# Optimization experiments

Measured on AMD Instinct MI355X. Metric: run time of the kernel, lower is better.

## Reference

```python
import jax, jax.numpy as jnp
import numpy as np

BS, QLEN, DIM, NH = 2, 2048, 1024, 16
HD = DIM // NH


def setup_inputs() -> dict:
    key = jax.random.key(0)
    ks = jax.random.split(key, 6)
    std = 0.02
    return {
        "x": jax.random.normal(ks[0], (BS, QLEN, DIM), dtype=jnp.float32),
        "mask": jnp.ones((BS, QLEN), dtype=jnp.float32),
        "Wq": jax.random.normal(ks[1], (DIM, DIM), dtype=jnp.float32) * std,
        "bq": jnp.zeros((DIM,), dtype=jnp.float32),
        "Wk": jax.random.normal(ks[2], (DIM, DIM), dtype=jnp.float32) * std,
        "bk": jnp.zeros((DIM,), dtype=jnp.float32),
        "Wv": jax.random.normal(ks[3], (DIM, DIM), dtype=jnp.float32) * std,
        "bv": jnp.zeros((DIM,), dtype=jnp.float32),
        "Wo": jax.random.normal(ks[4], (DIM, DIM), dtype=jnp.float32) * std,
        "bo": jnp.zeros((DIM,), dtype=jnp.float32),
    }


def reference(x, mask, Wq, bq, Wk, bk, Wv, bv, Wo, bo):
    bs, qlen, dim = x.shape
    # project and split heads: [bs, nh, len, hd]
    def split_heads(t):
        return t.reshape(bs, -1, NH, HD).transpose(0, 2, 1, 3)

    q = split_heads(x @ Wq + bq) / jnp.sqrt(jnp.float32(HD))
    k = split_heads(x @ Wk + bk)
    v = split_heads(x @ Wv + bv)

    scores = jnp.einsum("bhqd,bhkd->bhqk", q, k)  # [bs, nh, qlen, klen]
    m = mask.reshape(bs, 1, 1, -1)  # 2D mask -> broadcast over heads and q
    scores = scores - 1e30 * (1.0 - m)
    weights = jax.nn.softmax(scores, axis=-1)
    # dropout p=0.0 at inference -> no-op; head_mask is None
    context = jnp.einsum("bhqk,bhkd->bhqd", weights, v)
    context = context.transpose(0, 2, 1, 3).reshape(bs, qlen, NH * HD)
    return context @ Wo + bo
```

## Files before the change

kernel.cpp:

```cpp
#include <hip/hip_runtime.h>
#include <stdint.h>

#define BSZ  2
#define SEQ  2048
#define DIM  1024
#define NHD  16
#define HD   64
#define MTOT (BSZ*SEQ)

using short8  = __attribute__((ext_vector_type(8))) short;
using floatx4 = __attribute__((ext_vector_type(4))) float;

#define QSCALE 0.18033688011112042f
#define BIGM   1.44e30f

__device__ __forceinline__ unsigned short f2bf(float f) {
    unsigned int u = __float_as_uint(f);
    u += 0x7fffu + ((u >> 16) & 1u);
    return (unsigned short)(u >> 16);
}
__device__ __forceinline__ unsigned int pk2r(float a, float b) {
    unsigned int ua = __float_as_uint(a) + 0x8000u;
    unsigned int ub = __float_as_uint(b) + 0x8000u;
    return __builtin_amdgcn_perm(ub, ua, 0x07060302);
}

__device__ __forceinline__ void gll16(const void* g, const void* lds) {
    unsigned int loff = (unsigned int)(unsigned long long)lds;
    __builtin_amdgcn_global_load_lds(
        (const __attribute__((address_space(1))) unsigned int*)g,
        (__attribute__((address_space(3))) unsigned int*)loff, 16, 0, 0);
}

__global__ __launch_bounds__(256)
void conv_x(const float* __restrict__ X, unsigned short* __restrict__ Xbf) {
    size_t i = ((size_t)blockIdx.x * 256 + threadIdx.x) * 8;
    float4 a = *(const float4*)(X + i);
    float4 b = *(const float4*)(X + i + 4);
    uint4 u = {pk2r(a.x, a.y), pk2r(a.z, a.w), pk2r(b.x, b.y), pk2r(b.z, b.w)};
    *(uint4*)(Xbf + i) = u;
}

__global__ __launch_bounds__(256)
void conv_wt(const float* __restrict__ Wq, const float* __restrict__ Wk,
             const float* __restrict__ Wv, const float* __restrict__ Wo,
             unsigned short* __restrict__ Wt3, unsigned short* __restrict__ Wto)
{
    __shared__ float tile[64 * 65];
    const int z = blockIdx.z;
    const float* W = (z == 0) ? Wq : (z == 1) ? Wk : (z == 2) ? Wv : Wo;
    unsigned short* out = (z < 3) ? (Wt3 + (size_t)z * DIM * DIM) : Wto;
    const int k0 = blockIdx.x * 64, n0 = blockIdx.y * 64;
    const int t = threadIdx.x;
    const int r = t >> 2, c0 = (t & 3) * 16;
#pragma unroll
    for (int j = 0; j < 4; ++j) {
        float4 v = *(const float4*)&W[(size_t)(k0 + r) * DIM + n0 + c0 + j * 4];
        tile[r * 65 + c0 + j * 4 + 0] = v.x;
        tile[r * 65 + c0 + j * 4 + 1] = v.y;
        tile[r * 65 + c0 + j * 4 + 2] = v.z;
        tile[r * 65 + c0 + j * 4 + 3] = v.w;
    }
    __syncthreads();
    unsigned int p[8];
#pragma unroll
    for (int j = 0; j < 8; ++j)
        p[j] = pk2r(tile[(c0 + 2 * j) * 65 + r], tile[(c0 + 2 * j + 1) * 65 + r]);
    uint4 u0 = {p[0], p[1], p[2], p[3]}, u1 = {p[4], p[5], p[6], p[7]};
    unsigned short* dst = out + (size_t)(n0 + r) * DIM + k0 + c0;
    *(uint4*)dst = u0;
    *(uint4*)(dst + 8) = u1;
}

__global__ __launch_bounds__(256)
void qkv_gemm(const unsigned short* __restrict__ Xbf,
              const unsigned short* __restrict__ Wt3,
              const float* __restrict__ bq, const float* __restrict__ bk,
              const float* __restrict__ bv,
              unsigned short* __restrict__ Qb,
              unsigned short* __restrict__ Kb,
              unsigned short* __restrict__ VbT)
{
    __shared__ unsigned short As[128 * 32];
    __shared__ unsigned short Bs[128 * 32];

    const int t = threadIdx.x, w = t >> 6, lane = t & 63;
    const int lm = lane & 15, grp = lane >> 4;
    const int wm = w >> 1, wn = w & 1;
    const int m0 = blockIdx.x * 128;
    const int mat = blockIdx.y >> 3;
    const int n0 = (blockIdx.y & 7) * 128;
    const unsigned short* Bg = Wt3 + (size_t)mat * DIM * DIM;

    const int lr = lane >> 2, lc = (lane & 3) * 8;

    floatx4 acc[4][4];
#pragma unroll
    for (int i = 0; i < 4; ++i)
#pragma unroll
        for (int j = 0; j < 4; ++j) acc[i][j] = (floatx4){0.f, 0.f, 0.f, 0.f};

    for (int kt = 0; kt < DIM / 32; ++kt) {
        const int k0 = kt * 32;
        const int r0 = w * 16;
        gll16(Xbf + (size_t)(m0 + r0 + lr) * DIM + k0 + lc,      &As[r0 * 32]);
        gll16(Xbf + (size_t)(m0 + 64 + r0 + lr) * DIM + k0 + lc, &As[(64 + r0) * 32]);
        gll16(Bg  + (size_t)(n0 + r0 + lr) * DIM + k0 + lc,      &Bs[r0 * 32]);
        gll16(Bg  + (size_t)(n0 + 64 + r0 + lr) * DIM + k0 + lc, &Bs[(64 + r0) * 32]);
        __syncthreads();
        short8 af[4], bf[4];
#pragma unroll
        for (int mt = 0; mt < 4; ++mt)
            af[mt] = *(const short8*)&As[(wm * 64 + mt * 16 + lm) * 32 + grp * 8];
#pragma unroll
        for (int nt = 0; nt < 4; ++nt)
            bf[nt] = *(const short8*)&Bs[(wn * 64 + nt * 16 + lm) * 32 + grp * 8];
#pragma unroll
        for (int mt = 0; mt < 4; ++mt)
#pragma unroll
            for (int nt = 0; nt < 4; ++nt)
                acc[mt][nt] = __builtin_amdgcn_mfma_f32_16x16x32_bf16(af[mt], bf[nt], acc[mt][nt], 0, 0, 0);
        __syncthreads();
    }

    if (mat == 2) {
#pragma unroll
        for (int nt = 0; nt < 4; ++nt) {
            const int c = n0 + wn * 64 + nt * 16 + lm;
            const float bb = bv[c];
            const int h = c >> 6, d = c & 63;
#pragma unroll
            for (int mt = 0; mt < 4; ++mt) {
                const int r = m0 + wm * 64 + mt * 16 + grp * 4;
                const int b = r >> 11, s = r & 2047;
                const int si = s & 63, sb = s & ~63;
                const int sphys = sb + ((((si >> 3) ^ (d & 7)) << 3) | (si & 7));
                uint2 pv;
                pv.x = pk2r(acc[mt][nt][0] + bb, acc[mt][nt][1] + bb);
                pv.y = pk2r(acc[mt][nt][2] + bb, acc[mt][nt][3] + bb);
                *(uint2*)&VbT[(((size_t)(b * NHD + h)) * HD + d) * SEQ + sphys] = pv;
            }
        }
    } else if (mat == 1) {
#pragma unroll
        for (int nt = 0; nt < 4; ++nt) {
            const int c = n0 + wn * 64 + nt * 16 + lm;
            const float bb = bk[c];
            const int h = c >> 6, d = c & 63;
#pragma unroll
            for (int mt = 0; mt < 4; ++mt)
#pragma unroll
                for (int reg = 0; reg < 4; ++reg) {
                    const int r = m0 + wm * 64 + mt * 16 + grp * 4 + reg;
                    const int b = r >> 11, s = r & 2047;
                    const int dphys = (((d >> 3) ^ (s & 7)) << 3) | (d & 7);
                    Kb[(((size_t)(b * NHD + h)) * SEQ + s) * HD + dphys] =
                        f2bf(acc[mt][nt][reg] + bb);
                }
        }
    } else {
#pragma unroll
        for (int nt = 0; nt < 4; ++nt) {
            const int c = n0 + wn * 64 + nt * 16 + lm;
            const float bb = bq[c];
            const int h = c >> 6, d = c & 63;
#pragma unroll
            for (int mt = 0; mt < 4; ++mt)
#pragma unroll
                for (int reg = 0; reg < 4; ++reg) {
                    const int r = m0 + wm * 64 + mt * 16 + grp * 4 + reg;
                    const int b = r >> 11, s = r & 2047;
                    Qb[(((size_t)(b * NHD + h)) * SEQ + s) * HD + d] =
                        f2bf((acc[mt][nt][reg] + bb) * QSCALE);
                }
        }
    }
}

__global__ __launch_bounds__(256)
void attn(const unsigned short* __restrict__ Qb,
          const unsigned short* __restrict__ Kb,
          const unsigned short* __restrict__ VbT,
          const float* __restrict__ mask,
          unsigned short* __restrict__ Cb)
{
    __shared__ unsigned short Kt[2][64 * 64];
    __shared__ unsigned short Vt[2][64 * 64];
    __shared__ unsigned short Ps[4][16 * 72];

    const int t = threadIdx.x, w = t >> 6, lane = t & 63;
    const int lm = lane & 15, grp = lane >> 4;
    const int x7 = lm & 7;
    const int bh = blockIdx.y, b = bh >> 4, h = bh & 15;
    const int q0 = blockIdx.x * 64;

    short8 qf[2];
    {
        const unsigned short* qrow = Qb + ((size_t)bh * SEQ + q0 + w * 16 + lm) * HD;
        qf[0] = *(const short8*)(qrow + grp * 8);
        qf[1] = *(const short8*)(qrow + 32 + grp * 8);
    }

    floatx4 oacc[4];
#pragma unroll
    for (int i = 0; i < 4; ++i) oacc[i] = (floatx4){0.f, 0.f, 0.f, 0.f};
    float lpart = 0.f;

    const unsigned short* Kg = Kb + (size_t)bh * SEQ * HD;
    const unsigned short* Vg = VbT + (size_t)bh * HD * SEQ;
    const int srow = lane >> 3, scol = (lane & 7) * 8;
    const float* maskb = mask + b * SEQ;
    unsigned short* Pw = &Ps[w][0];

    {
        gll16(Kg + (size_t)(0 * 64 + w * 16 + srow) * HD + scol,     &Kt[0][(w * 16) * 64]);
        gll16(Kg + (size_t)(0 * 64 + w * 16 + 8 + srow) * HD + scol, &Kt[0][(w * 16 + 8) * 64]);
        gll16(Vg + (size_t)(w * 16 + srow) * SEQ + 0 * 64 + scol,     &Vt[0][(w * 16) * 64]);
        gll16(Vg + (size_t)(w * 16 + 8 + srow) * SEQ + 0 * 64 + scol, &Vt[0][(w * 16 + 8) * 64]);
    }

    for (int kt = 0; kt < SEQ / 64; ++kt) {
        const int cur = kt & 1;
        __syncthreads();
        if (kt + 1 < SEQ / 64) {
            const int nxt = cur ^ 1, kn = kt + 1;
            gll16(Kg + (size_t)(kn * 64 + w * 16 + srow) * HD + scol,     &Kt[nxt][(w * 16) * 64]);
            gll16(Kg + (size_t)(kn * 64 + w * 16 + 8 + srow) * HD + scol, &Kt[nxt][(w * 16 + 8) * 64]);
            gll16(Vg + (size_t)(w * 16 + srow) * SEQ + kn * 64 + scol,     &Vt[nxt][(w * 16) * 64]);
            gll16(Vg + (size_t)(w * 16 + 8 + srow) * SEQ + kn * 64 + scol, &Vt[nxt][(w * 16 + 8) * 64]);
        }

        floatx4 sv[4];
#pragma unroll
        for (int cg = 0; cg < 4; ++cg) {
            short8 a0 = *(const short8*)&Kt[cur][(cg * 16 + lm) * 64 + ((grp    ) ^ x7) * 8];
            short8 a1 = *(const short8*)&Kt[cur][(cg * 16 + lm) * 64 + ((4 + grp) ^ x7) * 8];
            floatx4 s = (floatx4){0.f, 0.f, 0.f, 0.f};
            s = __builtin_amdgcn_mfma_f32_16x16x32_bf16(a0, qf[0], s, 0, 0, 0);
            s = __builtin_amdgcn_mfma_f32_16x16x32_bf16(a1, qf[1], s, 0, 0, 0);
            sv[cg] = s;
        }

#pragma unroll
        for (int cg = 0; cg < 4; ++cg) {
            float4 mv = *(const float4*)&maskb[kt * 64 + cg * 16 + grp * 4];
            float p0 = __builtin_exp2f(sv[cg][0] + __builtin_fmaf(mv.x, BIGM, -BIGM));
            float p1 = __builtin_exp2f(sv[cg][1] + __builtin_fmaf(mv.y, BIGM, -BIGM));
            float p2 = __builtin_exp2f(sv[cg][2] + __builtin_fmaf(mv.z, BIGM, -BIGM));
            float p3 = __builtin_exp2f(sv[cg][3] + __builtin_fmaf(mv.w, BIGM, -BIGM));
            lpart += (p0 + p1) + (p2 + p3);
            uint2 pk;
            pk.x = pk2r(p0, p1);
            pk.y = pk2r(p2, p3);
            *(uint2*)&Pw[lm * 72 + cg * 16 + grp * 4] = pk;
        }

#pragma unroll
        for (int s2 = 0; s2 < 2; ++s2) {
            short8 ap = *(const short8*)&Pw[lm * 72 + s2 * 32 + grp * 8];
#pragma unroll
            for (int dg = 0; dg < 4; ++dg) {
                short8 bv2 = *(const short8*)&Vt[cur][(dg * 16 + lm) * 64 + ((s2 * 4 + grp) ^ x7) * 8];
                oacc[dg] = __builtin_amdgcn_mfma_f32_16x16x32_bf16(ap, bv2, oacc[dg], 0, 0, 0);
            }
        }
    }

    lpart += __shfl_xor(lpart, 16);
    lpart += __shfl_xor(lpart, 32);
    const float linv = (lpart > 0.f) ? 1.0f / lpart : 0.f;
    float inv[4];
#pragma unroll
    for (int r = 0; r < 4; ++r) inv[r] = __shfl(linv, grp * 4 + r);
#pragma unroll
    for (int dg = 0; dg < 4; ++dg)
#pragma unroll
        for (int r = 0; r < 4; ++r) {
            const int s = q0 + w * 16 + grp * 4 + r;
            Cb[((size_t)(b * SEQ + s)) * DIM + h * HD + dg * 16 + lm] =
                f2bf(oacc[dg][r] * inv[r]);
        }
}

__global__ __launch_bounds__(256)
void out_gemm(const unsigned short* __restrict__ Cb,
              const unsigned short* __restrict__ Wto,
              const float* __restrict__ bo,
              float* __restrict__ out)
{
    __shared__ unsigned short As[128 * 32];
    __shared__ unsigned short Bs[64 * 32];

    const int t = threadIdx.x, w = t >> 6, lane = t & 63;
    const int lm = lane & 15, grp = lane >> 4;
    const int m0 = blockIdx.x * 128;
    const int n0 = blockIdx.y * 64;

    const int lr = lane >> 2, lc = (lane & 3) * 8;

    floatx4 acc[2][4];
#pragma unroll
    for (int i = 0; i < 2; ++i)
#pragma unroll
        for (int j = 0; j < 4; ++j) acc[i][j] = (floatx4){0.f, 0.f, 0.f, 0.f};

    for (int kt = 0; kt < DIM / 32; ++kt) {
        const int k0 = kt * 32;
        const int r0 = w * 16;
        gll16(Cb  + (size_t)(m0 + r0 + lr) * DIM + k0 + lc,      &As[r0 * 32]);
        gll16(Cb  + (size_t)(m0 + 64 + r0 + lr) * DIM + k0 + lc, &As[(64 + r0) * 32]);
        gll16(Wto + (size_t)(n0 + r0 + lr) * DIM + k0 + lc,      &Bs[r0 * 32]);
        __syncthreads();
        short8 af[2], bf[4];
#pragma unroll
        for (int mt = 0; mt < 2; ++mt)
            af[mt] = *(const short8*)&As[(w * 32 + mt * 16 + lm) * 32 + grp * 8];
#pragma unroll
        for (int nt = 0; nt < 4; ++nt)
            bf[nt] = *(const short8*)&Bs[(nt * 16 + lm) * 32 + grp * 8];
#pragma unroll
        for (int mt = 0; mt < 2; ++mt)
#pragma unroll
            for (int nt = 0; nt < 4; ++nt)
                acc[mt][nt] = __builtin_amdgcn_mfma_f32_16x16x32_bf16(af[mt], bf[nt], acc[mt][nt], 0, 0, 0);
        __syncthreads();
    }

#pragma unroll
    for (int nt = 0; nt < 4; ++nt) {
        const int c = n0 + nt * 16 + lm;
        const float bb = bo[c];
#pragma unroll
        for (int mt = 0; mt < 2; ++mt)
#pragma unroll
            for (int reg = 0; reg < 4; ++reg) {
                const int r = m0 + w * 32 + mt * 16 + grp * 4 + reg;
                out[(size_t)r * DIM + c] = acc[mt][nt][reg] + bb;
            }
    }
}

extern "C" void kernel_launch(void* const* d_in, const int* in_sizes, int n_in,
                              void* d_out, int out_size, void* d_ws, size_t ws_size,
                              hipStream_t stream)
{
    const float* x    = (const float*)d_in[0];
    const float* mask = (const float*)d_in[1];
    const float* Wq   = (const float*)d_in[2];
    const float* bq   = (const float*)d_in[3];
    const float* Wk   = (const float*)d_in[4];
    const float* bk   = (const float*)d_in[5];
    const float* Wv   = (const float*)d_in[6];
    const float* bv   = (const float*)d_in[7];
    const float* Wo   = (const float*)d_in[8];
    const float* bo   = (const float*)d_in[9];
    float* out = (float*)d_out;

    const size_t M1 = (size_t)DIM * DIM;
    unsigned short* Qb  = (unsigned short*)d_ws;
    unsigned short* Kb  = Qb  + 4 * M1;
    unsigned short* VbT = Kb  + 4 * M1;
    unsigned short* Cb  = VbT + 4 * M1;
    unsigned short* Xbf = Cb  + 4 * M1;
    unsigned short* Wt3 = Xbf + 4 * M1;
    unsigned short* Wto = Wt3 + 3 * M1;

    conv_x <<<dim3((MTOT * DIM) / 2048), 256, 0, stream>>>(x, Xbf);
    conv_wt<<<dim3(16, 16, 4), 256, 0, stream>>>(Wq, Wk, Wv, Wo, Wt3, Wto);
    qkv_gemm<<<dim3(MTOT / 128, 24), 256, 0, stream>>>(Xbf, Wt3, bq, bk, bv, Qb, Kb, VbT);
    attn<<<dim3(SEQ / 64, BSZ * NHD), 256, 0, stream>>>(Qb, Kb, VbT, mask, Cb);
    out_gemm<<<dim3(MTOT / 128, DIM / 64), 256, 0, stream>>>(Cb, Wto, bo, out);
}
```

Baseline: 237.1 us.

## Split attention key range across waves and drop LDS K/V staging

The attention kernel now gives each wave a quarter of the key sequence for all 64 queries, instead of giving each wave 16 queries over the full sequence. K and V fragments are loaded straight from global memory into registers rather than double-buffered through swizzled LDS, and the partial outputs and row sums are reduced across waves through LDS at the end. The K/V swizzles in the projection kernel are removed to match. This removes the per-tile barriers and LDS traffic but raises register pressure (16 output accumulators plus K/V fragments) and depends on uncoalesced direct global loads hitting cache.

```diff
diff --git a/kernel.cpp b/kernel.cpp
--- a/kernel.cpp
+++ b/kernel.cpp
@@ -133,12 +133,10 @@
             for (int mt = 0; mt < 4; ++mt) {
                 const int r = m0 + wm * 64 + mt * 16 + grp * 4;
                 const int b = r >> 11, s = r & 2047;
-                const int si = s & 63, sb = s & ~63;
-                const int sphys = sb + ((((si >> 3) ^ (d & 7)) << 3) | (si & 7));
                 uint2 pv;
                 pv.x = pk2r(acc[mt][nt][0] + bb, acc[mt][nt][1] + bb);
                 pv.y = pk2r(acc[mt][nt][2] + bb, acc[mt][nt][3] + bb);
-                *(uint2*)&VbT[(((size_t)(b * NHD + h)) * HD + d) * SEQ + sphys] = pv;
+                *(uint2*)&VbT[(((size_t)(b * NHD + h)) * HD + d) * SEQ + s] = pv;
             }
         }
     } else if (mat == 1) {
@@ -153,8 +151,7 @@
                 for (int reg = 0; reg < 4; ++reg) {
                     const int r = m0 + wm * 64 + mt * 16 + grp * 4 + reg;
                     const int b = r >> 11, s = r & 2047;
-                    const int dphys = (((d >> 3) ^ (s & 7)) << 3) | (d & 7);
-                    Kb[(((size_t)(b * NHD + h)) * SEQ + s) * HD + dphys] =
+                    Kb[(((size_t)(b * NHD + h)) * SEQ + s) * HD + d] =
                         f2bf(acc[mt][nt][reg] + bb);
                 }
         }
@@ -184,102 +181,143 @@
           const float* __restrict__ mask,
           unsigned short* __restrict__ Cb)
 {
-    __shared__ unsigned short Kt[2][64 * 64];
-    __shared__ unsigned short Vt[2][64 * 64];
-    __shared__ unsigned short Ps[4][16 * 72];
+    __shared__ union {
+        unsigned short Ps[4][64 * 72];
+        struct { float Oex[12][16 * 66]; float Lex[4][64]; } ep;
+    } sm;
 
     const int t = threadIdx.x, w = t >> 6, lane = t & 63;
     const int lm = lane & 15, grp = lane >> 4;
-    const int x7 = lm & 7;
     const int bh = blockIdx.y, b = bh >> 4, h = bh & 15;
     const int q0 = blockIdx.x * 64;
 
-    short8 qf[2];
-    {
-        const unsigned short* qrow = Qb + ((size_t)bh * SEQ + q0 + w * 16 + lm) * HD;
-        qf[0] = *(const short8*)(qrow + grp * 8);
-        qf[1] = *(const short8*)(qrow + 32 + grp * 8);
-    }
-
-    floatx4 oacc[4];
-#pragma unroll
-    for (int i = 0; i < 4; ++i) oacc[i] = (floatx4){0.f, 0.f, 0.f, 0.f};
-    float lpart = 0.f;
+    short8 qf[4][2];
+#pragma unroll
+    for (int qt = 0; qt < 4; ++qt) {
+        const unsigned short* qrow = Qb + ((size_t)bh * SEQ + q0 + qt * 16 + lm) * HD;
+        qf[qt][0] = *(const short8*)(qrow + grp * 8);
+        qf[qt][1] = *(const short8*)(qrow + 32 + grp * 8);
+    }
+
+    floatx4 oacc[4][4];
+#pragma unroll
+    for (int i = 0; i < 4; ++i)
+#pragma unroll
+        for (int j = 0; j < 4; ++j) oacc[i][j] = (floatx4){0.f, 0.f, 0.f, 0.f};
+    float lpart[4] = {0.f, 0.f, 0.f, 0.f};
 
     const unsigned short* Kg = Kb + (size_t)bh * SEQ * HD;
     const unsigned short* Vg = VbT + (size_t)bh * HD * SEQ;
-    const int srow = lane >> 3, scol = (lane & 7) * 8;
     const float* maskb = mask + b * SEQ;
-    unsigned short* Pw = &Ps[w][0];
-
-    {
-        gll16(Kg + (size_t)(0 * 64 + w * 16 + srow) * HD + scol,     &Kt[0][(w * 16) * 64]);
-        gll16(Kg + (size_t)(0 * 64 + w * 16 + 8 + srow) * HD + scol, &Kt[0][(w * 16 + 8) * 64]);
-        gll16(Vg + (size_t)(w * 16 + srow) * SEQ + 0 * 64 + scol,     &Vt[0][(w * 16) * 64]);
-        gll16(Vg + (size_t)(w * 16 + 8 + srow) * SEQ + 0 * 64 + scol, &Vt[0][(w * 16 + 8) * 64]);
-    }
-
-    for (int kt = 0; kt < SEQ / 64; ++kt) {
-        const int cur = kt & 1;
-        __syncthreads();
-        if (kt + 1 < SEQ / 64) {
-            const int nxt = cur ^ 1, kn = kt + 1;
-            gll16(Kg + (size_t)(kn * 64 + w * 16 + srow) * HD + scol,     &Kt[nxt][(w * 16) * 64]);
-            gll16(Kg + (size_t)(kn * 64 + w * 16 + 8 + srow) * HD + scol, &Kt[nxt][(w * 16 + 8) * 64]);
-            gll16(Vg + (size_t)(w * 16 + srow) * SEQ + kn * 64 + scol,     &Vt[nxt][(w * 16) * 64]);
-            gll16(Vg + (size_t)(w * 16 + 8 + srow) * SEQ + kn * 64 + scol, &Vt[nxt][(w * 16 + 8) * 64]);
-        }
-
-        floatx4 sv[4];
+    unsigned short* Pw = sm.Ps[w];
+
+    for (int kt = 0; kt < 8; ++kt) {
+        const int kb = w * 512 + kt * 64;
+
+        short8 kf[4][2], vf[4][2];
 #pragma unroll
         for (int cg = 0; cg < 4; ++cg) {
-            short8 a0 = *(const short8*)&Kt[cur][(cg * 16 + lm) * 64 + ((grp    ) ^ x7) * 8];
-            short8 a1 = *(const short8*)&Kt[cur][(cg * 16 + lm) * 64 + ((4 + grp) ^ x7) * 8];
-            floatx4 s = (floatx4){0.f, 0.f, 0.f, 0.f};
-            s = __builtin_amdgcn_mfma_f32_16x16x32_bf16(a0, qf[0], s, 0, 0, 0);
-            s = __builtin_amdgcn_mfma_f32_16x16x32_bf16(a1, qf[1], s, 0, 0, 0);
-            sv[cg] = s;
+            const unsigned short* kr = Kg + (size_t)(kb + cg * 16 + lm) * HD;
+            kf[cg][0] = *(const short8*)(kr + grp * 8);
+            kf[cg][1] = *(const short8*)(kr + 32 + grp * 8);
+        }
+#pragma unroll
+        for (int dg = 0; dg < 4; ++dg) {
+            const unsigned short* vr = Vg + (size_t)(dg * 16 + lm) * SEQ + kb;
+            vf[dg][0] = *(const short8*)(vr + grp * 8);
+            vf[dg][1] = *(const short8*)(vr + 32 + grp * 8);
         }
 
 #pragma unroll
         for (int cg = 0; cg < 4; ++cg) {
-            float4 mv = *(const float4*)&maskb[kt * 64 + cg * 16 + grp * 4];
-            float p0 = __builtin_exp2f(sv[cg][0] + __builtin_fmaf(mv.x, BIGM, -BIGM));
-            float p1 = __builtin_exp2f(sv[cg][1] + __builtin_fmaf(mv.y, BIGM, -BIGM));
-            float p2 = __builtin_exp2f(sv[cg][2] + __builtin_fmaf(mv.z, BIGM, -BIGM));
-            float p3 = __builtin_exp2f(sv[cg][3] + __builtin_fmaf(mv.w, BIGM, -BIGM));
-            lpart += (p0 + p1) + (p2 + p3);
-            uint2 pk;
-            pk.x = pk2r(p0, p1);
-            pk.y = pk2r(p2, p3);
-            *(uint2*)&Pw[lm * 72 + cg * 16 + grp * 4] = pk;
-        }
-
-#pragma unroll
-        for (int s2 = 0; s2 < 2; ++s2) {
-            short8 ap = *(const short8*)&Pw[lm * 72 + s2 * 32 + grp * 8];
+            float4 mv = *(const float4*)&maskb[kb + cg * 16 + grp * 4];
+            const float m0a = __builtin_fmaf(mv.x, BIGM, -BIGM);
+            const float m1a = __builtin_fmaf(mv.y, BIGM, -BIGM);
+            const float m2a = __builtin_fmaf(mv.z, BIGM, -BIGM);
+            const float m3a = __builtin_fmaf(mv.w, BIGM, -BIGM);
+#pragma unroll
+            for (int qt = 0; qt < 4; ++qt) {
+                floatx4 s = (floatx4){0.f, 0.f, 0.f, 0.f};
+                s = __builtin_amdgcn_mfma_f32_16x16x32_bf16(kf[cg][0], qf[qt][0], s, 0, 0, 0);
+                s = __builtin_amdgcn_mfma_f32_16x16x32_bf16(kf[cg][1], qf[qt][1], s, 0, 0, 0);
+                float p0 = __builtin_exp2f(s[0] + m0a);
+                float p1 = __builtin_exp2f(s[1] + m1a);
+                float p2 = __builtin_exp2f(s[2] + m2a);
+                float p3 = __builtin_exp2f(s[3] + m3a);
+                lpart[qt] += (p0 + p1) + (p2 + p3);
+                uint2 pk;
+                pk.x = pk2r(p0, p1);
+                pk.y = pk2r(p2, p3);
+                *(uint2*)&Pw[(qt * 16 + lm) * 72 + cg * 16 + grp * 4] = pk;
+            }
+        }
+
+#pragma unroll
+        for (int qt = 0; qt < 4; ++qt) {
+            short8 ap0 = *(const short8*)&Pw[(qt * 16 + lm) * 72 + grp * 8];
+            short8 ap1 = *(const short8*)&Pw[(qt * 16 + lm) * 72 + 32 + grp * 8];
 #pragma unroll
             for (int dg = 0; dg < 4; ++dg) {
-                short8 bv2 = *(const short8*)&Vt[cur][(dg * 16 + lm) * 64 + ((s2 * 4 + grp) ^ x7) * 8];
-                oacc[dg] = __builtin_amdgcn_mfma_f32_16x16x32_bf16(ap, bv2, oacc[dg], 0, 0, 0);
+                oacc[qt][dg] = __builtin_amdgcn_mfma_f32_16x16x32_bf16(ap0, vf[dg][0], oacc[qt][dg], 0, 0, 0);
+                oacc[qt][dg] = __builtin_amdgcn_mfma_f32_16x16x32_bf16(ap1, vf[dg][1], oacc[qt][dg], 0, 0, 0);
             }
         }
     }
 
-    lpart += __shfl_xor(lpart, 16);
-    lpart += __shfl_xor(lpart, 32);
-    const float linv = (lpart > 0.f) ? 1.0f / lpart : 0.f;
+    float lred[4];
+#pragma unroll
+    for (int qt = 0; qt < 4; ++qt) {
+        float l = lpart[qt];
+        l += __shfl_xor(l, 16);
+        l += __shfl_xor(l, 32);
+        lred[qt] = l;
+    }
+
+    __syncthreads();
+
+#pragma unroll
+    for (int qt = 0; qt < 4; ++qt) {
+        if (qt != w) {
+            const int slot = qt * 3 + (w > qt ? w - 1 : w);
+            float* T = sm.ep.Oex[slot];
+#pragma unroll
+            for (int dg = 0; dg < 4; ++dg)
+#pragma unroll
+                for (int r = 0; r < 4; ++r)
+                    T[(grp * 4 + r) * 66 + dg * 16 + lm] = oacc[qt][dg][r];
+        }
+    }
+    if (grp == 0) {
+#pragma unroll
+        for (int qt = 0; qt < 4; ++qt)
+            sm.ep.Lex[w][qt * 16 + lm] = lred[qt];
+    }
+    __syncthreads();
+
+    float lt = sm.ep.Lex[0][w * 16 + lm] + sm.ep.Lex[1][w * 16 + lm]
+             + sm.ep.Lex[2][w * 16 + lm] + sm.ep.Lex[3][w * 16 + lm];
+    const float li = (lt > 0.f) ? 1.0f / lt : 0.f;
     float inv[4];
 #pragma unroll
-    for (int r = 0; r < 4; ++r) inv[r] = __shfl(linv, grp * 4 + r);
-#pragma unroll
-    for (int dg = 0; dg < 4; ++dg)
-#pragma unroll
-        for (int r = 0; r < 4; ++r) {
-            const int s = q0 + w * 16 + grp * 4 + r;
-            Cb[((size_t)(b * SEQ + s)) * DIM + h * HD + dg * 16 + lm] =
-                f2bf(oacc[dg][r] * inv[r]);
-        }
+    for (int r = 0; r < 4; ++r) inv[r] = __shfl(li, grp * 4 + r);
+
+#pragma unroll
+    for (int qt = 0; qt < 4; ++qt) {
+        if (qt == w) {
+#pragma unroll
+            for (int dg = 0; dg < 4; ++dg)
+#pragma unroll
+                for (int r = 0; r < 4; ++r) {
+                    float v = oacc[qt][dg][r];
+#pragma unroll
+                    for (int j = 0; j < 3; ++j)
+                        v += sm.ep.Oex[w * 3 + j][(grp * 4 + r) * 66 + dg * 16 + lm];
+                    const int s = q0 + w * 16 + grp * 4 + r;
+                    Cb[((size_t)(b * SEQ + s)) * DIM + h * HD + dg * 16 + lm] =
+                        f2bf(v * inv[r]);
+                }
+        }
+    }
 }
 
 __global__ __launch_bounds__(256)
```

Measured after the change: 285.1 us. +20.2%, slower.

## Load K/V fragments directly from global memory into registers in attention

Applied to the files above, without the earlier changes.

Removes the double-buffered LDS staging of K and V tiles and the block-wide barrier per key tile. Each wave now reads its K and V MFMA fragments straight from global memory (relying on L1/L2 reuse across the four waves), and the XOR swizzle in the projection stores is dropped to match. Launch bounds add an occupancy hint of 4 blocks. This trades LDS traffic and synchronisation for redundant global/cache loads by each wave and less explicit prefetch overlap.

```diff
diff --git a/kernel.cpp b/kernel.cpp
--- a/kernel.cpp
+++ b/kernel.cpp
@@ -133,12 +133,10 @@
             for (int mt = 0; mt < 4; ++mt) {
                 const int r = m0 + wm * 64 + mt * 16 + grp * 4;
                 const int b = r >> 11, s = r & 2047;
-                const int si = s & 63, sb = s & ~63;
-                const int sphys = sb + ((((si >> 3) ^ (d & 7)) << 3) | (si & 7));
                 uint2 pv;
                 pv.x = pk2r(acc[mt][nt][0] + bb, acc[mt][nt][1] + bb);
                 pv.y = pk2r(acc[mt][nt][2] + bb, acc[mt][nt][3] + bb);
-                *(uint2*)&VbT[(((size_t)(b * NHD + h)) * HD + d) * SEQ + sphys] = pv;
+                *(uint2*)&VbT[(((size_t)(b * NHD + h)) * HD + d) * SEQ + s] = pv;
             }
         }
     } else if (mat == 1) {
@@ -153,8 +151,7 @@
                 for (int reg = 0; reg < 4; ++reg) {
                     const int r = m0 + wm * 64 + mt * 16 + grp * 4 + reg;
                     const int b = r >> 11, s = r & 2047;
-                    const int dphys = (((d >> 3) ^ (s & 7)) << 3) | (d & 7);
-                    Kb[(((size_t)(b * NHD + h)) * SEQ + s) * HD + dphys] =
+                    Kb[(((size_t)(b * NHD + h)) * SEQ + s) * HD + d] =
                         f2bf(acc[mt][nt][reg] + bb);
                 }
         }
@@ -177,20 +174,17 @@
     }
 }
 
-__global__ __launch_bounds__(256)
+__global__ __launch_bounds__(256, 4)
 void attn(const unsigned short* __restrict__ Qb,
           const unsigned short* __restrict__ Kb,
           const unsigned short* __restrict__ VbT,
           const float* __restrict__ mask,
           unsigned short* __restrict__ Cb)
 {
-    __shared__ unsigned short Kt[2][64 * 64];
-    __shared__ unsigned short Vt[2][64 * 64];
     __shared__ unsigned short Ps[4][16 * 72];
 
     const int t = threadIdx.x, w = t >> 6, lane = t & 63;
     const int lm = lane & 15, grp = lane >> 4;
-    const int x7 = lm & 7;
     const int bh = blockIdx.y, b = bh >> 4, h = bh & 15;
     const int q0 = blockIdx.x * 64;
 
@@ -208,46 +202,41 @@
 
     const unsigned short* Kg = Kb + (size_t)bh * SEQ * HD;
     const unsigned short* Vg = VbT + (size_t)bh * HD * SEQ;
-    const int srow = lane >> 3, scol = (lane & 7) * 8;
     const float* maskb = mask + b * SEQ;
-    unsigned short* Pw = &Ps[w][0];
-
-    {
-        gll16(Kg + (size_t)(0 * 64 + w * 16 + srow) * HD + scol,     &Kt[0][(w * 16) * 64]);
-        gll16(Kg + (size_t)(0 * 64 + w * 16 + 8 + srow) * HD + scol, &Kt[0][(w * 16 + 8) * 64]);
-        gll16(Vg + (size_t)(w * 16 + srow) * SEQ + 0 * 64 + scol,     &Vt[0][(w * 16) * 64]);
-        gll16(Vg + (size_t)(w * 16 + 8 + srow) * SEQ + 0 * 64 + scol, &Vt[0][(w * 16 + 8) * 64]);
-    }
-
+    unsigned short* Pw = Ps[w];
+
+#pragma unroll 1
     for (int kt = 0; kt < SEQ / 64; ++kt) {
-        const int cur = kt & 1;
-        __syncthreads();
-        if (kt + 1 < SEQ / 64) {
-            const int nxt = cur ^ 1, kn = kt + 1;
-            gll16(Kg + (size_t)(kn * 64 + w * 16 + srow) * HD + scol,     &Kt[nxt][(w * 16) * 64]);
-            gll16(Kg + (size_t)(kn * 64 + w * 16 + 8 + srow) * HD + scol, &Kt[nxt][(w * 16 + 8) * 64]);
-            gll16(Vg + (size_t)(w * 16 + srow) * SEQ + kn * 64 + scol,     &Vt[nxt][(w * 16) * 64]);
-            gll16(Vg + (size_t)(w * 16 + 8 + srow) * SEQ + kn * 64 + scol, &Vt[nxt][(w * 16 + 8) * 64]);
-        }
-
-        floatx4 sv[4];
+        const int kb = kt * 64;
+
+        short8 kf[4][2];
 #pragma unroll
         for (int cg = 0; cg < 4; ++cg) {
-            short8 a0 = *(const short8*)&Kt[cur][(cg * 16 + lm) * 64 + ((grp    ) ^ x7) * 8];
-            short8 a1 = *(const short8*)&Kt[cur][(cg * 16 + lm) * 64 + ((4 + grp) ^ x7) * 8];
+            const unsigned short* kr = Kg + (size_t)(kb + cg * 16 + lm) * HD;
+            kf[cg][0] = *(const short8*)(kr + grp * 8);
+            kf[cg][1] = *(const short8*)(kr + 32 + grp * 8);
+        }
+        float4 mv[4];
+#pragma unroll
+        for (int cg = 0; cg < 4; ++cg)
+            mv[cg] = *(const float4*)&maskb[kb + cg * 16 + grp * 4];
+        short8 vf[4][2];
+#pragma unroll
+        for (int dg = 0; dg < 4; ++dg) {
+            const unsigned short* vr = Vg + (size_t)(dg * 16 + lm) * SEQ + kb;
+            vf[dg][0] = *(const short8*)(vr + grp * 8);
+            vf[dg][1] = *(const short8*)(vr + 32 + grp * 8);
+        }
+
+#pragma unroll
+        for (int cg = 0; cg < 4; ++cg) {
             floatx4 s = (floatx4){0.f, 0.f, 0.f, 0.f};
-            s = __builtin_amdgcn_mfma_f32_16x16x32_bf16(a0, qf[0], s, 0, 0, 0);
-            s = __builtin_amdgcn_mfma_f32_16x16x32_bf16(a1, qf[1], s, 0, 0, 0);
-            sv[cg] = s;
-        }
-
-#pragma unroll
-        for (int cg = 0; cg < 4; ++cg) {
-            float4 mv = *(const float4*)&maskb[kt * 64 + cg * 16 + grp * 4];
-            float p0 = __builtin_exp2f(sv[cg][0] + __builtin_fmaf(mv.x, BIGM, -BIGM));
-            float p1 = __builtin_exp2f(sv[cg][1] + __builtin_fmaf(mv.y, BIGM, -BIGM));
-            float p2 = __builtin_exp2f(sv[cg][2] + __builtin_fmaf(mv.z, BIGM, -BIGM));
-            float p3 = __builtin_exp2f(sv[cg][3] + __builtin_fmaf(mv.w, BIGM, -BIGM));
+            s = __builtin_amdgcn_mfma_f32_16x16x32_bf16(kf[cg][0], qf[0], s, 0, 0, 0);
+            s = __builtin_amdgcn_mfma_f32_16x16x32_bf16(kf[cg][1], qf[1], s, 0, 0, 0);
+            float p0 = __builtin_exp2f(s[0] + __builtin_fmaf(mv[cg].x, BIGM, -BIGM));
+            float p1 = __builtin_exp2f(s[1] + __builtin_fmaf(mv[cg].y, BIGM, -BIGM));
+            float p2 = __builtin_exp2f(s[2] + __builtin_fmaf(mv[cg].z, BIGM, -BIGM));
+            float p3 = __builtin_exp2f(s[3] + __builtin_fmaf(mv[cg].w, BIGM, -BIGM));
             lpart += (p0 + p1) + (p2 + p3);
             uint2 pk;
             pk.x = pk2r(p0, p1);
@@ -259,10 +248,8 @@
         for (int s2 = 0; s2 < 2; ++s2) {
             short8 ap = *(const short8*)&Pw[lm * 72 + s2 * 32 + grp * 8];
 #pragma unroll
-            for (int dg = 0; dg < 4; ++dg) {
-                short8 bv2 = *(const short8*)&Vt[cur][(dg * 16 + lm) * 64 + ((s2 * 4 + grp) ^ x7) * 8];
-                oacc[dg] = __builtin_amdgcn_mfma_f32_16x16x32_bf16(ap, bv2, oacc[dg], 0, 0, 0);
-            }
+            for (int dg = 0; dg < 4; ++dg)
+                oacc[dg] = __builtin_amdgcn_mfma_f32_16x16x32_bf16(ap, vf[dg][s2], oacc[dg], 0, 0, 0);
         }
     }
 
```

After: 401.6 us. 1.69x slower.

## Keep softmax probabilities in registers by permuting V layout to match MFMA operands

Applied to the files above, without the earlier changes.

The V-transpose writer now permutes sequence positions inside each 64-block so the bf16 probabilities produced by the QK MFMA can be fed directly as the A operand of the PV MFMA. This removes the per-wave LDS round trip for P. The mask is also precomputed into an additive LDS array once per block, and the launch bounds request 4 blocks per CU. The change relies on the k-permutation being applied consistently to both P and V, and it adds register pressure from holding the V fragments.

```diff
diff --git a/kernel.cpp b/kernel.cpp
--- a/kernel.cpp
+++ b/kernel.cpp
@@ -134,11 +134,13 @@
                 const int r = m0 + wm * 64 + mt * 16 + grp * 4;
                 const int b = r >> 11, s = r & 2047;
                 const int si = s & 63, sb = s & ~63;
-                const int sphys = sb + ((((si >> 3) ^ (d & 7)) << 3) | (si & 7));
+                const int cg = si >> 4, g = (si >> 2) & 3;
+                const int unit = (((cg & 1) << 2) | g) ^ (d & 7);
+                const int sph = sb + unit * 8 + ((cg >> 1) << 2);
                 uint2 pv;
                 pv.x = pk2r(acc[mt][nt][0] + bb, acc[mt][nt][1] + bb);
                 pv.y = pk2r(acc[mt][nt][2] + bb, acc[mt][nt][3] + bb);
-                *(uint2*)&VbT[(((size_t)(b * NHD + h)) * HD + d) * SEQ + sphys] = pv;
+                *(uint2*)&VbT[(((size_t)(b * NHD + h)) * HD + d) * SEQ + sph] = pv;
             }
         }
     } else if (mat == 1) {
@@ -177,7 +179,7 @@
     }
 }
 
-__global__ __launch_bounds__(256)
+__global__ __launch_bounds__(256, 4)
 void attn(const unsigned short* __restrict__ Qb,
           const unsigned short* __restrict__ Kb,
           const unsigned short* __restrict__ VbT,
@@ -186,7 +188,7 @@
 {
     __shared__ unsigned short Kt[2][64 * 64];
     __shared__ unsigned short Vt[2][64 * 64];
-    __shared__ unsigned short Ps[4][16 * 72];
+    __shared__ float Msk[SEQ];
 
     const int t = threadIdx.x, w = t >> 6, lane = t & 63;
     const int lm = lane & 15, grp = lane >> 4;
@@ -201,6 +203,19 @@
         qf[1] = *(const short8*)(qrow + 32 + grp * 8);
     }
 
+    {
+        const float* mb = mask + b * SEQ;
+        const int i = t * 8;
+        float4 a = *(const float4*)(mb + i);
+        float4 c = *(const float4*)(mb + i + 4);
+        float4 ra = {__builtin_fmaf(a.x, BIGM, -BIGM), __builtin_fmaf(a.y, BIGM, -BIGM),
+                     __builtin_fmaf(a.z, BIGM, -BIGM), __builtin_fmaf(a.w, BIGM, -BIGM)};
+        float4 rc = {__builtin_fmaf(c.x, BIGM, -BIGM), __builtin_fmaf(c.y, BIGM, -BIGM),
+                     __builtin_fmaf(c.z, BIGM, -BIGM), __builtin_fmaf(c.w, BIGM, -BIGM)};
+        *(float4*)&Msk[i]     = ra;
+        *(float4*)&Msk[i + 4] = rc;
+    }
+
     floatx4 oacc[4];
 #pragma unroll
     for (int i = 0; i < 4; ++i) oacc[i] = (floatx4){0.f, 0.f, 0.f, 0.f};
@@ -209,25 +224,23 @@
     const unsigned short* Kg = Kb + (size_t)bh * SEQ * HD;
     const unsigned short* Vg = VbT + (size_t)bh * HD * SEQ;
     const int srow = lane >> 3, scol = (lane & 7) * 8;
-    const float* maskb = mask + b * SEQ;
-    unsigned short* Pw = &Ps[w][0];
-
-    {
-        gll16(Kg + (size_t)(0 * 64 + w * 16 + srow) * HD + scol,     &Kt[0][(w * 16) * 64]);
-        gll16(Kg + (size_t)(0 * 64 + w * 16 + 8 + srow) * HD + scol, &Kt[0][(w * 16 + 8) * 64]);
-        gll16(Vg + (size_t)(w * 16 + srow) * SEQ + 0 * 64 + scol,     &Vt[0][(w * 16) * 64]);
-        gll16(Vg + (size_t)(w * 16 + 8 + srow) * SEQ + 0 * 64 + scol, &Vt[0][(w * 16 + 8) * 64]);
-    }
-
+
+    gll16(Kg + (size_t)(w * 16 + srow) * HD + scol,      &Kt[0][(w * 16) * 64]);
+    gll16(Kg + (size_t)(w * 16 + 8 + srow) * HD + scol,  &Kt[0][(w * 16 + 8) * 64]);
+    gll16(Vg + (size_t)(w * 16 + srow) * SEQ + scol,     &Vt[0][(w * 16) * 64]);
+    gll16(Vg + (size_t)(w * 16 + 8 + srow) * SEQ + scol, &Vt[0][(w * 16 + 8) * 64]);
+
+#pragma unroll 1
     for (int kt = 0; kt < SEQ / 64; ++kt) {
         const int cur = kt & 1;
+        const int kb = kt * 64;
         __syncthreads();
         if (kt + 1 < SEQ / 64) {
-            const int nxt = cur ^ 1, kn = kt + 1;
-            gll16(Kg + (size_t)(kn * 64 + w * 16 + srow) * HD + scol,     &Kt[nxt][(w * 16) * 64]);
-            gll16(Kg + (size_t)(kn * 64 + w * 16 + 8 + srow) * HD + scol, &Kt[nxt][(w * 16 + 8) * 64]);
-            gll16(Vg + (size_t)(w * 16 + srow) * SEQ + kn * 64 + scol,     &Vt[nxt][(w * 16) * 64]);
-            gll16(Vg + (size_t)(w * 16 + 8 + srow) * SEQ + kn * 64 + scol, &Vt[nxt][(w * 16 + 8) * 64]);
+            const int nxt = cur ^ 1, kn = (kt + 1) * 64;
+            gll16(Kg + (size_t)(kn + w * 16 + srow) * HD + scol,      &Kt[nxt][(w * 16) * 64]);
+            gll16(Kg + (size_t)(kn + w * 16 + 8 + srow) * HD + scol,  &Kt[nxt][(w * 16 + 8) * 64]);
+            gll16(Vg + (size_t)(w * 16 + srow) * SEQ + kn + scol,     &Vt[nxt][(w * 16) * 64]);
+            gll16(Vg + (size_t)(w * 16 + 8 + srow) * SEQ + kn + scol, &Vt[nxt][(w * 16 + 8) * 64]);
         }
 
         floatx4 sv[4];
@@ -241,28 +254,36 @@
             sv[cg] = s;
         }
 
+        short8 vf[4][2];
+#pragma unroll
+        for (int dg = 0; dg < 4; ++dg) {
+            vf[dg][0] = *(const short8*)&Vt[cur][(dg * 16 + lm) * 64 + ((grp    ) ^ x7) * 8];
+            vf[dg][1] = *(const short8*)&Vt[cur][(dg * 16 + lm) * 64 + ((4 + grp) ^ x7) * 8];
+        }
+
+        float p[4][4];
 #pragma unroll
         for (int cg = 0; cg < 4; ++cg) {
-            float4 mv = *(const float4*)&maskb[kt * 64 + cg * 16 + grp * 4];
-            float p0 = __builtin_exp2f(sv[cg][0] + __builtin_fmaf(mv.x, BIGM, -BIGM));
-            float p1 = __builtin_exp2f(sv[cg][1] + __builtin_fmaf(mv.y, BIGM, -BIGM));
-            float p2 = __builtin_exp2f(sv[cg][2] + __builtin_fmaf(mv.z, BIGM, -BIGM));
-            float p3 = __builtin_exp2f(sv[cg][3] + __builtin_fmaf(mv.w, BIGM, -BIGM));
-            lpart += (p0 + p1) + (p2 + p3);
-            uint2 pk;
-            pk.x = pk2r(p0, p1);
-            pk.y = pk2r(p2, p3);
-            *(uint2*)&Pw[lm * 72 + cg * 16 + grp * 4] = pk;
-        }
-
-#pragma unroll
-        for (int s2 = 0; s2 < 2; ++s2) {
-            short8 ap = *(const short8*)&Pw[lm * 72 + s2 * 32 + grp * 8];
-#pragma unroll
-            for (int dg = 0; dg < 4; ++dg) {
-                short8 bv2 = *(const short8*)&Vt[cur][(dg * 16 + lm) * 64 + ((s2 * 4 + grp) ^ x7) * 8];
-                oacc[dg] = __builtin_amdgcn_mfma_f32_16x16x32_bf16(ap, bv2, oacc[dg], 0, 0, 0);
-            }
+            float4 md = *(const float4*)&Msk[kb + cg * 16 + grp * 4];
+            p[cg][0] = __builtin_exp2f(sv[cg][0] + md.x);
+            p[cg][1] = __builtin_exp2f(sv[cg][1] + md.y);
+            p[cg][2] = __builtin_exp2f(sv[cg][2] + md.z);
+            p[cg][3] = __builtin_exp2f(sv[cg][3] + md.w);
+            lpart += (p[cg][0] + p[cg][1]) + (p[cg][2] + p[cg][3]);
+        }
+
+        uint4 u0, u1;
+        u0.x = pk2r(p[0][0], p[0][1]); u0.y = pk2r(p[0][2], p[0][3]);
+        u0.z = pk2r(p[2][0], p[2][1]); u0.w = pk2r(p[2][2], p[2][3]);
+        u1.x = pk2r(p[1][0], p[1][1]); u1.y = pk2r(p[1][2], p[1][3]);
+        u1.z = pk2r(p[3][0], p[3][1]); u1.w = pk2r(p[3][2], p[3][3]);
+        short8 ap0 = *(const short8*)&u0;
+        short8 ap1 = *(const short8*)&u1;
+
+#pragma unroll
+        for (int dg = 0; dg < 4; ++dg) {
+            oacc[dg] = __builtin_amdgcn_mfma_f32_16x16x32_bf16(ap0, vf[dg][0], oacc[dg], 0, 0, 0);
+            oacc[dg] = __builtin_amdgcn_mfma_f32_16x16x32_bf16(ap1, vf[dg][1], oacc[dg], 0, 0, 0);
         }
     }
 
```

Result: faster. 218.1 us (-8.0%).
